# Kernel tuning notes

Measured on AMD Instinct MI355X. Metric: run time of the kernel, lower is better.

The kernel has to match this reference:

```python
import jax, jax.numpy as jnp
import numpy as np

N, S, E, H, P = 8, 384, 768, 12, 384
D = E // H


def setup_inputs() -> dict:
    rng = jax.random.key(0)
    ks = jax.random.split(rng, 20)
    w = lambda k, shape: jax.random.normal(k, shape, dtype=jnp.float32) * 0.02
    return {
        "value": jax.random.normal(ks[0], (N, S, E), dtype=jnp.float32),
        "key": jax.random.normal(ks[1], (N, S, E), dtype=jnp.float32),
        "query": jax.random.normal(ks[2], (N, S, E), dtype=jnp.float32),
        "mask": jnp.ones((N, 1, 1, S), dtype=jnp.int32),
        "Wq": w(ks[3], (E, E)), "bq": jnp.zeros((E,), jnp.float32),
        "Wkc": w(ks[4], (E, E)), "bkc": jnp.zeros((E,), jnp.float32),
        "Wkp": w(ks[5], (E, E)), "bkp": jnp.zeros((E,), jnp.float32),
        "Wv": w(ks[6], (E, E)), "bv": jnp.zeros((E,), jnp.float32),
        "Wfc": w(ks[7], (E, E)), "bfc": jnp.zeros((E,), jnp.float32),
        "pos_emb": w(ks[8], (2 * P, E)),
    }


def reference(value, key, query, mask, Wq, bq, Wkc, bkc, Wkp, bkp, Wv, bv, Wfc, bfc, pos_emb):
    n, q_len, e = query.shape
    h, d = H, E // H
    # relative position ids in [0, 2P)
    pos_ids = jnp.arange(q_len)
    rel = pos_ids[None, :] - pos_ids[:, None] + P          # [Q, Q]
    pe = pos_emb[rel]                                       # [Q, Q, E]

    qh = (query @ Wq.T + bq).reshape(n, q_len, h, d)        # nqhd
    kc = (key @ Wkc.T + bkc).reshape(n, q_len, h, d)        # nkhd
    kp = (pe @ Wkp.T + bkp).reshape(q_len, q_len, h, d)     # qkhd
    v = (value @ Wv.T + bv).reshape(n, q_len, h, d)         # nkhd

    scores = jnp.einsum('nqhd,nkhd->nhqk', qh, kc) \
           + jnp.einsum('nqhd,qkhd->nhqk', qh, kp)
    scores = jnp.where(mask == 0, -jnp.inf, scores)
    attn = jax.nn.softmax(scores / (e ** 0.5), axis=-1)     # [N,H,Q,K]

    out = jnp.einsum('nhqk,nkhd->nqhd', attn, v).reshape(n, q_len, e)
    out = out @ Wfc.T + bfc
    return (out, attn)
```

## Files before the change

### kernel.cpp

```cpp
#include <hip/hip_runtime.h>
#include <hip/hip_bf16.h>
#include <math.h>

#define NBATCH 8
#define SEQ    384
#define EMB    768
#define NH     12
#define HD     64
#define PP     384
#define RELN   768

#define INV_SQRT_E 0.036084391824351615f

typedef __attribute__((ext_vector_type(8))) short bf16x8;
typedef __attribute__((ext_vector_type(4))) float f32x4;

__device__ inline void cvt8(const float4 a, const float4 b, bf16x8& h8, bf16x8& l8)
{
    const float f[8] = {a.x, a.y, a.z, a.w, b.x, b.y, b.z, b.w};
    #pragma unroll
    for (int j = 0; j < 8; ++j) {
        __hip_bfloat16 hb = __float2bfloat16(f[j]);
        const float r = f[j] - __bfloat162float(hb);
        __hip_bfloat16 lb = __float2bfloat16(r);
        h8[j] = *reinterpret_cast<const short*>(&hb);
        l8[j] = *reinterpret_cast<const short*>(&lb);
    }
}

__global__ __launch_bounds__(256) void gemm_bf16x2(
    const float* __restrict__ A, const float* __restrict__ B,
    const float* __restrict__ bias, float* __restrict__ C,
    int M, int N, int K)
{
    __shared__ __align__(16) __hip_bfloat16 sAh[128 * 32];
    __shared__ __align__(16) __hip_bfloat16 sAl[128 * 32];
    __shared__ __align__(16) __hip_bfloat16 sBh[64 * 32];
    __shared__ __align__(16) __hip_bfloat16 sBl[64 * 32];

    const int tid  = threadIdx.x;
    const int bm   = blockIdx.y * 128;
    const int bn   = blockIdx.x * 64;
    const int wave = tid >> 6;
    const int lane = tid & 63;
    const int wm   = wave >> 1;
    const int wn   = wave & 1;
    const int fr   = lane & 15;
    const int fg   = lane >> 4;

    const int rowS = tid >> 2;
    const int kOfs = (tid & 3) * 8;

    const float* Ap0 = A + (size_t)(bm + rowS) * K + kOfs;
    const float* Ap1 = A + (size_t)(bm + rowS + 64) * K + kOfs;
    const float* Bp  = B + (size_t)(bn + rowS) * K + kOfs;

    float4 a0a = *reinterpret_cast<const float4*>(Ap0);
    float4 a0b = *reinterpret_cast<const float4*>(Ap0 + 4);
    float4 a1a = *reinterpret_cast<const float4*>(Ap1);
    float4 a1b = *reinterpret_cast<const float4*>(Ap1 + 4);
    float4 bba = *reinterpret_cast<const float4*>(Bp);
    float4 bbb = *reinterpret_cast<const float4*>(Bp + 4);

    f32x4 acc[4][2];
    #pragma unroll
    for (int i = 0; i < 4; ++i)
        #pragma unroll
        for (int j = 0; j < 2; ++j)
            acc[i][j] = (f32x4){0.f, 0.f, 0.f, 0.f};

    const int ldsA = rowS * 32 + kOfs;
    const int ldsB = rowS * 32 + kOfs;

    for (int k0 = 0; k0 < K; k0 += 32) {
        __syncthreads();
        {
            bf16x8 h8, l8;
            cvt8(a0a, a0b, h8, l8);
            *reinterpret_cast<bf16x8*>(&sAh[ldsA]) = h8;
            *reinterpret_cast<bf16x8*>(&sAl[ldsA]) = l8;
            cvt8(a1a, a1b, h8, l8);
            *reinterpret_cast<bf16x8*>(&sAh[ldsA + 64 * 32]) = h8;
            *reinterpret_cast<bf16x8*>(&sAl[ldsA + 64 * 32]) = l8;
            cvt8(bba, bbb, h8, l8);
            *reinterpret_cast<bf16x8*>(&sBh[ldsB]) = h8;
            *reinterpret_cast<bf16x8*>(&sBl[ldsB]) = l8;
        }
        __syncthreads();

        if (k0 + 32 < K) {
            a0a = *reinterpret_cast<const float4*>(Ap0 + k0 + 32);
            a0b = *reinterpret_cast<const float4*>(Ap0 + k0 + 36);
            a1a = *reinterpret_cast<const float4*>(Ap1 + k0 + 32);
            a1b = *reinterpret_cast<const float4*>(Ap1 + k0 + 36);
            bba = *reinterpret_cast<const float4*>(Bp  + k0 + 32);
            bbb = *reinterpret_cast<const float4*>(Bp  + k0 + 36);
        }

        bf16x8 fah[4], fal[4], fbh[2], fbl[2];
        #pragma unroll
        for (int mf = 0; mf < 4; ++mf) {
            const int row = wm * 64 + mf * 16 + fr;
            fah[mf] = *reinterpret_cast<const bf16x8*>(&sAh[row * 32 + fg * 8]);
            fal[mf] = *reinterpret_cast<const bf16x8*>(&sAl[row * 32 + fg * 8]);
        }
        #pragma unroll
        for (int nf = 0; nf < 2; ++nf) {
            const int col = wn * 32 + nf * 16 + fr;
            fbh[nf] = *reinterpret_cast<const bf16x8*>(&sBh[col * 32 + fg * 8]);
            fbl[nf] = *reinterpret_cast<const bf16x8*>(&sBl[col * 32 + fg * 8]);
        }

        #pragma unroll
        for (int mf = 0; mf < 4; ++mf)
            #pragma unroll
            for (int nf = 0; nf < 2; ++nf) {
                acc[mf][nf] = __builtin_amdgcn_mfma_f32_16x16x32_bf16(fah[mf], fbh[nf], acc[mf][nf], 0, 0, 0);
                acc[mf][nf] = __builtin_amdgcn_mfma_f32_16x16x32_bf16(fah[mf], fbl[nf], acc[mf][nf], 0, 0, 0);
                acc[mf][nf] = __builtin_amdgcn_mfma_f32_16x16x32_bf16(fal[mf], fbh[nf], acc[mf][nf], 0, 0, 0);
            }
    }

    #pragma unroll
    for (int nf = 0; nf < 2; ++nf) {
        const int col = bn + wn * 32 + nf * 16 + fr;
        const float bb = bias[col];
        #pragma unroll
        for (int mf = 0; mf < 4; ++mf) {
            #pragma unroll
            for (int reg = 0; reg < 4; ++reg) {
                const int row = bm + wm * 64 + mf * 16 + fg * 4 + reg;
                C[(size_t)row * N + col] = acc[mf][nf][reg] + bb;
            }
        }
    }
}

#define QT32  32
#define KT    64
#define NKT   (SEQ / KT)
#define NRT   7
#define BUFP  68
#define SCP   392

__global__ __launch_bounds__(256) void fused_attn(
    const float* __restrict__ qh, const float* __restrict__ kc,
    const float* __restrict__ kp, const float* __restrict__ v,
    const int* __restrict__ mask,
    float* __restrict__ attn, float* __restrict__ ctx)
{
    __shared__ float qs[QT32][BUFP];
    __shared__ float sc[QT32][SCP];
    __shared__ float buf[KT][BUFP];
    __shared__ float rowinv[QT32];

    const int bid  = blockIdx.x;
    const int tile = bid % (SEQ / QT32);
    const int h    = (bid / (SEQ / QT32)) % NH;
    const int n    = bid / ((SEQ / QT32) * NH);
    const int q0   = tile * QT32;
    const int tid  = threadIdx.x;
    const int tqg  = tid >> 4;
    const int tkg  = tid & 15;

    #pragma unroll
    for (int i = 0; i < 2; ++i) {
        const int idx = tid + i * 256;
        const int row = idx >> 4;
        const int seg = idx & 15;
        *reinterpret_cast<float4*>(&qs[row][seg * 4]) =
            *reinterpret_cast<const float4*>(&qh[((size_t)(n * SEQ + q0 + row) * NH + h) * HD + seg * 4]);
    }

    for (int kt = 0; kt < NKT; ++kt) {
        __syncthreads();
        #pragma unroll
        for (int i = 0; i < 4; ++i) {
            const int idx = tid + i * 256;
            const int row = idx >> 4;
            const int seg = idx & 15;
            *reinterpret_cast<float4*>(&buf[row][seg * 4]) =
                *reinterpret_cast<const float4*>(&kc[((size_t)(n * SEQ + kt * KT + row) * NH + h) * HD + seg * 4]);
        }
        __syncthreads();

        float acc[2][4] = {};
        #pragma unroll
        for (int d4 = 0; d4 < 16; ++d4) {
            const float4 qa = *reinterpret_cast<const float4*>(&qs[2 * tqg + 0][d4 * 4]);
            const float4 qb = *reinterpret_cast<const float4*>(&qs[2 * tqg + 1][d4 * 4]);
            #pragma unroll
            for (int j = 0; j < 4; ++j) {
                const float4 kv = *reinterpret_cast<const float4*>(&buf[tkg + 16 * j][d4 * 4]);
                acc[0][j] += qa.x * kv.x + qa.y * kv.y + qa.z * kv.z + qa.w * kv.w;
                acc[1][j] += qb.x * kv.x + qb.y * kv.y + qb.z * kv.z + qb.w * kv.w;
            }
        }
        #pragma unroll
        for (int j = 0; j < 4; ++j) {
            sc[2 * tqg + 0][kt * KT + tkg + 16 * j] = acc[0][j];
            sc[2 * tqg + 1][kt * KT + tkg + 16 * j] = acc[1][j];
        }
    }

    const int rstart = PP - q0 - (QT32 - 1);
    for (int rt = 0; rt < NRT; ++rt) {
        __syncthreads();
        #pragma unroll
        for (int i = 0; i < 4; ++i) {
            const int idx = tid + i * 256;
            const int row = idx >> 4;
            const int seg = idx & 15;
            int r = rstart + rt * KT + row;
            if (r > RELN - 1) r = RELN - 1;
            *reinterpret_cast<float4*>(&buf[row][seg * 4]) =
                *reinterpret_cast<const float4*>(&kp[(size_t)r * EMB + h * HD + seg * 4]);
        }
        __syncthreads();

        float g[2][4] = {};
        #pragma unroll
        for (int d4 = 0; d4 < 16; ++d4) {
            const float4 qa = *reinterpret_cast<const float4*>(&qs[2 * tqg + 0][d4 * 4]);
            const float4 qb = *reinterpret_cast<const float4*>(&qs[2 * tqg + 1][d4 * 4]);
            #pragma unroll
            for (int j = 0; j < 4; ++j) {
                const float4 kv = *reinterpret_cast<const float4*>(&buf[tkg + 16 * j][d4 * 4]);
                g[0][j] += qa.x * kv.x + qa.y * kv.y + qa.z * kv.z + qa.w * kv.w;
                g[1][j] += qb.x * kv.x + qb.y * kv.y + qb.z * kv.z + qb.w * kv.w;
            }
        }
        #pragma unroll
        for (int i = 0; i < 2; ++i) {
            const int qq = 2 * tqg + i;
            #pragma unroll
            for (int j = 0; j < 4; ++j) {
                const int rloc = rt * KT + tkg + 16 * j;
                const int k = qq - (QT32 - 1) + rloc;
                if (k >= 0 && k < SEQ) sc[qq][k] += g[i][j];
            }
        }
    }
    __syncthreads();

    const int srow  = tid >> 3;
    const int slane = tid & 7;

    float m = -INFINITY;
    for (int c = slane; c < SEQ; c += 8) {
        const float raw = sc[srow][c];
        const float val = (mask[n * SEQ + c] == 0) ? -INFINITY : raw * INV_SQRT_E;
        m = fmaxf(m, val);
    }
    #pragma unroll
    for (int off = 1; off < 8; off <<= 1) m = fmaxf(m, __shfl_xor(m, off));

    float ssum = 0.f;
    for (int c = slane; c < SEQ; c += 8) {
        const float raw = sc[srow][c];
        const float val = (mask[n * SEQ + c] == 0) ? -INFINITY : raw * INV_SQRT_E;
        const float e = __expf(val - m);
        sc[srow][c] = e;
        ssum += e;
    }
    #pragma unroll
    for (int off = 1; off < 8; off <<= 1) ssum += __shfl_xor(ssum, off);
    if (slane == 0) rowinv[srow] = 1.f / ssum;
    __syncthreads();

    float* attn_base = attn + ((size_t)(n * NH + h) * SEQ + q0) * SEQ;
    for (int idx = tid; idx < QT32 * SEQ; idx += 256) {
        const int row = idx / SEQ;
        const int col = idx - row * SEQ;
        const float p = sc[row][col] * rowinv[row];
        sc[row][col] = p;
        attn_base[(size_t)row * SEQ + col] = p;
    }

    float cacc[2][4] = {};
    for (int kt = 0; kt < NKT; ++kt) {
        __syncthreads();
        #pragma unroll
        for (int i = 0; i < 4; ++i) {
            const int idx = tid + i * 256;
            const int row = idx >> 4;
            const int seg = idx & 15;
            *reinterpret_cast<float4*>(&buf[row][seg * 4]) =
                *reinterpret_cast<const float4*>(&v[((size_t)(n * SEQ + kt * KT + row) * NH + h) * HD + seg * 4]);
        }
        __syncthreads();

        for (int kk = 0; kk < KT; ++kk) {
            const float pa = sc[2 * tqg + 0][kt * KT + kk];
            const float pb = sc[2 * tqg + 1][kt * KT + kk];
            const float4 vv = *reinterpret_cast<const float4*>(&buf[kk][tkg * 4]);
            cacc[0][0] += pa * vv.x; cacc[0][1] += pa * vv.y;
            cacc[0][2] += pa * vv.z; cacc[0][3] += pa * vv.w;
            cacc[1][0] += pb * vv.x; cacc[1][1] += pb * vv.y;
            cacc[1][2] += pb * vv.z; cacc[1][3] += pb * vv.w;
        }
    }
    #pragma unroll
    for (int i = 0; i < 2; ++i) {
        float4 o;
        o.x = cacc[i][0]; o.y = cacc[i][1]; o.z = cacc[i][2]; o.w = cacc[i][3];
        *reinterpret_cast<float4*>(
            &ctx[((size_t)(n * SEQ + q0 + 2 * tqg + i) * NH + h) * HD + tkg * 4]) = o;
    }
}

extern "C" void kernel_launch(void* const* d_in, const int* in_sizes, int n_in,
                              void* d_out, int out_size, void* d_ws, size_t ws_size,
                              hipStream_t stream)
{
    const float* value  = (const float*)d_in[0];
    const float* key    = (const float*)d_in[1];
    const float* query  = (const float*)d_in[2];
    const int*   mask   = (const int*)  d_in[3];
    const float* Wq     = (const float*)d_in[4];
    const float* bq     = (const float*)d_in[5];
    const float* Wkc    = (const float*)d_in[6];
    const float* bkc    = (const float*)d_in[7];
    const float* Wkp    = (const float*)d_in[8];
    const float* bkp    = (const float*)d_in[9];
    const float* Wv     = (const float*)d_in[10];
    const float* bv     = (const float*)d_in[11];
    const float* Wfc    = (const float*)d_in[12];
    const float* bfc    = (const float*)d_in[13];
    const float* pos_emb = (const float*)d_in[14];

    float* out  = (float*)d_out;
    float* attn = (float*)d_out + (size_t)NBATCH * SEQ * EMB;

    float* ws  = (float*)d_ws;
    float* qh  = ws;
    float* kc  = qh + (size_t)NBATCH * SEQ * EMB;
    float* v   = kc + (size_t)NBATCH * SEQ * EMB;
    float* kp  = v  + (size_t)NBATCH * SEQ * EMB;
    float* ctx = kp + (size_t)RELN * EMB;

    const int M1 = NBATCH * SEQ;

    dim3 gblk(256);
    dim3 ggrid(EMB / 64, M1 / 128);
    dim3 ggrid_p(EMB / 64, RELN / 128);

    gemm_bf16x2<<<ggrid,   gblk, 0, stream>>>(query,   Wq,  bq,  qh, M1,   EMB, EMB);
    gemm_bf16x2<<<ggrid,   gblk, 0, stream>>>(key,     Wkc, bkc, kc, M1,   EMB, EMB);
    gemm_bf16x2<<<ggrid,   gblk, 0, stream>>>(value,   Wv,  bv,  v,  M1,   EMB, EMB);
    gemm_bf16x2<<<ggrid_p, gblk, 0, stream>>>(pos_emb, Wkp, bkp, kp, RELN, EMB, EMB);

    fused_attn<<<NBATCH * NH * (SEQ / QT32), 256, 0, stream>>>(qh, kc, kp, v, mask, attn, ctx);

    gemm_bf16x2<<<ggrid, gblk, 0, stream>>>(ctx, Wfc, bfc, out, M1, EMB, EMB);
}
```

Baseline: 630.7 us.

## Register-prefetch next K/Kp/V tiles, cache mask in LDS, vectorize attn store

Loads of the next kc, kp and v tile are issued into registers before the current tile's compute, so global-load latency overlaps the shared-memory dot products. The mask row is staged once in shared memory instead of being re-read from global memory in both softmax passes. The probability normalization and attention write now use float4 accesses. The cost is extra registers per thread (12 float4 prefetch buffers), which could lower occupancy.

```diff
diff --git a/kernel.cpp b/kernel.cpp
--- a/kernel.cpp
+++ b/kernel.cpp
@@ -153,6 +153,7 @@
     __shared__ float sc[QT32][SCP];
     __shared__ float buf[KT][BUFP];
     __shared__ float rowinv[QT32];
+    __shared__ int   smask[SEQ];
 
     const int bid  = blockIdx.x;
     const int tile = bid % (SEQ / QT32);
@@ -171,16 +172,27 @@
         *reinterpret_cast<float4*>(&qs[row][seg * 4]) =
             *reinterpret_cast<const float4*>(&qh[((size_t)(n * SEQ + q0 + row) * NH + h) * HD + seg * 4]);
     }
+    for (int i = tid; i < SEQ; i += 256) smask[i] = mask[n * SEQ + i];
+
+    const int r0   = tid >> 4;
+    const int seg4 = (tid & 15) * 4;
+
+    const float* kcbase = kc + ((size_t)(n * SEQ) * NH + h) * HD;
+    float4 pfa[4];
+    #pragma unroll
+    for (int i = 0; i < 4; ++i)
+        pfa[i] = *reinterpret_cast<const float4*>(kcbase + (size_t)(r0 + 16 * i) * EMB + seg4);
 
     for (int kt = 0; kt < NKT; ++kt) {
         __syncthreads();
         #pragma unroll
-        for (int i = 0; i < 4; ++i) {
-            const int idx = tid + i * 256;
-            const int row = idx >> 4;
-            const int seg = idx & 15;
-            *reinterpret_cast<float4*>(&buf[row][seg * 4]) =
-                *reinterpret_cast<const float4*>(&kc[((size_t)(n * SEQ + kt * KT + row) * NH + h) * HD + seg * 4]);
+        for (int i = 0; i < 4; ++i)
+            *reinterpret_cast<float4*>(&buf[r0 + 16 * i][seg4]) = pfa[i];
+        if (kt + 1 < NKT) {
+            #pragma unroll
+            for (int i = 0; i < 4; ++i)
+                pfa[i] = *reinterpret_cast<const float4*>(
+                    kcbase + (size_t)((kt + 1) * KT + r0 + 16 * i) * EMB + seg4);
         }
         __syncthreads();
 
@@ -204,17 +216,27 @@
     }
 
     const int rstart = PP - q0 - (QT32 - 1);
+    const float* kpbase = kp + h * HD;
+    float4 pfb[4];
+    #pragma unroll
+    for (int i = 0; i < 4; ++i) {
+        int r = rstart + r0 + 16 * i;
+        if (r > RELN - 1) r = RELN - 1;
+        pfb[i] = *reinterpret_cast<const float4*>(kpbase + (size_t)r * EMB + seg4);
+    }
+
     for (int rt = 0; rt < NRT; ++rt) {
         __syncthreads();
         #pragma unroll
-        for (int i = 0; i < 4; ++i) {
-            const int idx = tid + i * 256;
-            const int row = idx >> 4;
-            const int seg = idx & 15;
-            int r = rstart + rt * KT + row;
-            if (r > RELN - 1) r = RELN - 1;
-            *reinterpret_cast<float4*>(&buf[row][seg * 4]) =
-                *reinterpret_cast<const float4*>(&kp[(size_t)r * EMB + h * HD + seg * 4]);
+        for (int i = 0; i < 4; ++i)
+            *reinterpret_cast<float4*>(&buf[r0 + 16 * i][seg4]) = pfb[i];
+        if (rt + 1 < NRT) {
+            #pragma unroll
+            for (int i = 0; i < 4; ++i) {
+                int r = rstart + (rt + 1) * KT + r0 + 16 * i;
+                if (r > RELN - 1) r = RELN - 1;
+                pfb[i] = *reinterpret_cast<const float4*>(kpbase + (size_t)r * EMB + seg4);
+            }
         }
         __syncthreads();
 
@@ -241,6 +263,13 @@
             }
         }
     }
+
+    const float* vbase = v + ((size_t)(n * SEQ) * NH + h) * HD;
+    float4 pfv[4];
+    #pragma unroll
+    for (int i = 0; i < 4; ++i)
+        pfv[i] = *reinterpret_cast<const float4*>(vbase + (size_t)(r0 + 16 * i) * EMB + seg4);
+
     __syncthreads();
 
     const int srow  = tid >> 3;
@@ -248,8 +277,7 @@
 
     float m = -INFINITY;
     for (int c = slane; c < SEQ; c += 8) {
-        const float raw = sc[srow][c];
-        const float val = (mask[n * SEQ + c] == 0) ? -INFINITY : raw * INV_SQRT_E;
+        const float val = (smask[c] == 0) ? -INFINITY : sc[srow][c] * INV_SQRT_E;
         m = fmaxf(m, val);
     }
     #pragma unroll
@@ -257,8 +285,7 @@
 
     float ssum = 0.f;
     for (int c = slane; c < SEQ; c += 8) {
-        const float raw = sc[srow][c];
-        const float val = (mask[n * SEQ + c] == 0) ? -INFINITY : raw * INV_SQRT_E;
+        const float val = (smask[c] == 0) ? -INFINITY : sc[srow][c] * INV_SQRT_E;
         const float e = __expf(val - m);
         sc[srow][c] = e;
         ssum += e;
@@ -269,24 +296,27 @@
     __syncthreads();
 
     float* attn_base = attn + ((size_t)(n * NH + h) * SEQ + q0) * SEQ;
-    for (int idx = tid; idx < QT32 * SEQ; idx += 256) {
-        const int row = idx / SEQ;
-        const int col = idx - row * SEQ;
-        const float p = sc[row][col] * rowinv[row];
-        sc[row][col] = p;
-        attn_base[(size_t)row * SEQ + col] = p;
+    for (int idx = tid; idx < QT32 * (SEQ / 4); idx += 256) {
+        const int row = idx / (SEQ / 4);
+        const int c4  = idx - row * (SEQ / 4);
+        float4 pv = *reinterpret_cast<float4*>(&sc[row][c4 * 4]);
+        const float inv = rowinv[row];
+        pv.x *= inv; pv.y *= inv; pv.z *= inv; pv.w *= inv;
+        *reinterpret_cast<float4*>(&sc[row][c4 * 4]) = pv;
+        *reinterpret_cast<float4*>(&attn_base[(size_t)row * SEQ + c4 * 4]) = pv;
     }
 
     float cacc[2][4] = {};
     for (int kt = 0; kt < NKT; ++kt) {
         __syncthreads();
         #pragma unroll
-        for (int i = 0; i < 4; ++i) {
-            const int idx = tid + i * 256;
-            const int row = idx >> 4;
-            const int seg = idx & 15;
-            *reinterpret_cast<float4*>(&buf[row][seg * 4]) =
-                *reinterpret_cast<const float4*>(&v[((size_t)(n * SEQ + kt * KT + row) * NH + h) * HD + seg * 4]);
+        for (int i = 0; i < 4; ++i)
+            *reinterpret_cast<float4*>(&buf[r0 + 16 * i][seg4]) = pfv[i];
+        if (kt + 1 < NKT) {
+            #pragma unroll
+            for (int i = 0; i < 4; ++i)
+                pfv[i] = *reinterpret_cast<const float4*>(
+                    vbase + (size_t)((kt + 1) * KT + r0 + 16 * i) * EMB + seg4);
         }
         __syncthreads();
 
```

After: 625.8 us. No clear change (-0.8%).
